# Performance work log

Measured on AMD Instinct MI355X. Metric: run time of the kernel, lower is better.

## Reference

```python
import jax, jax.numpy as jnp
import numpy as np

B, S, DIM = 2, 2048, 2048
NH = 16
Q_LORA, KV_LORA = 1536, 512
NOPE, ROPE, VHD = 128, 64, 128
QK_HD = NOPE + ROPE  # 192
EPS = 1e-6
SCALE = QK_HD ** -0.5


def rmsnorm(x, w, eps=EPS):
    return x * jax.lax.rsqrt(jnp.mean(x * x, axis=-1, keepdims=True) + eps) * w


def apply_rope(x, cos, sin):
    # x: (b, s, h, d) with d even; cos/sin: (s, d//2)
    xr, xi = x[..., 0::2], x[..., 1::2]
    c = cos[None, :, None, :]
    s = sin[None, :, None, :]
    yr = xr * c - xi * s
    yi = xr * s + xi * c
    return jnp.stack([yr, yi], axis=-1).reshape(x.shape)


def setup_inputs() -> dict:
    key = jax.random.key(0)
    ks = jax.random.split(key, 12)
    std = 0.02
    # RoPE tables (unit-magnitude complex as cos/sin)
    inv_freq = 1.0 / (10000.0 ** (np.arange(0, ROPE, 2, dtype=np.float32) / ROPE))  # (32,)
    ang = np.arange(S, dtype=np.float32)[:, None] * inv_freq[None, :]  # (S, 32)
    return {
        "x": jax.random.normal(ks[0], (B, S, DIM), jnp.float32),
        "freqs_cos": jnp.asarray(np.cos(ang)),
        "freqs_sin": jnp.asarray(np.sin(ang)),
        "wq_a_w": jax.random.normal(ks[1], (Q_LORA, DIM), jnp.float32) * std,
        "wq_a_b": jnp.zeros((Q_LORA,), jnp.float32),
        "q_norm_w": jnp.ones((Q_LORA,), jnp.float32),
        "wq_b_w": jax.random.normal(ks[2], (NH * QK_HD, Q_LORA), jnp.float32) * std,
        "wq_b_b": jnp.zeros((NH * QK_HD,), jnp.float32),
        "wkv_a_w": jax.random.normal(ks[3], (KV_LORA + ROPE, DIM), jnp.float32) * std,
        "wkv_a_b": jnp.zeros((KV_LORA + ROPE,), jnp.float32),
        "kv_norm_w": jnp.ones((KV_LORA,), jnp.float32),
        "wkv_b_w": jax.random.normal(ks[4], (NH * (NOPE + VHD), KV_LORA), jnp.float32) * std,
        "wkv_b_b": jnp.zeros((NH * (NOPE + VHD),), jnp.float32),
        "wo_w": jax.random.normal(ks[5], (DIM, NH * VHD), jnp.float32) * std,
        "wo_b": jnp.zeros((DIM,), jnp.float32),
    }


def reference(x, freqs_cos, freqs_sin, wq_a_w, wq_a_b, q_norm_w, wq_b_w, wq_b_b,
              wkv_a_w, wkv_a_b, kv_norm_w, wkv_b_w, wkv_b_b, wo_w, wo_b):
    b, s, _ = x.shape
    # Low-rank Q projection: wq_b(q_norm(wq_a(x)))
    q = rmsnorm(x @ wq_a_w.T + wq_a_b, q_norm_w) @ wq_b_w.T + wq_b_b
    q = q.reshape(b, s, NH, QK_HD)
    q_nope, q_pe = q[..., :NOPE], q[..., NOPE:]
    q = jnp.concatenate([q_nope, apply_rope(q_pe, freqs_cos, freqs_sin)], axis=-1)
    # Low-rank KV projection
    kv = x @ wkv_a_w.T + wkv_a_b  # (b, s, kv_lora + rope)
    kv_c, k_pe = kv[..., :KV_LORA], kv[..., KV_LORA:]
    k_pe = apply_rope(k_pe[:, :, None, :], freqs_cos, freqs_sin)  # (b, s, 1, rope)
    kv = rmsnorm(kv_c, kv_norm_w) @ wkv_b_w.T + wkv_b_b
    kv = kv.reshape(b, s, NH, NOPE + VHD)
    k_nope, v = kv[..., :NOPE], kv[..., NOPE:]
    k = jnp.concatenate([k_nope, jnp.broadcast_to(k_pe, (b, s, NH, ROPE))], axis=-1)
    # Causal SDPA
    scores = jnp.einsum("bqhd,bkhd->bhqk", q, k) * SCALE
    causal = jnp.tril(jnp.ones((s, s), bool))
    scores = jnp.where(causal[None, None], scores, jnp.float32(-1e30))
    attn = jax.nn.softmax(scores, axis=-1)
    out = jnp.einsum("bhqk,bkhd->bqhd", attn, v).reshape(b, s, NH * VHD)
    return out @ wo_w.T + wo_b
```

## Files before the change

kernel.cpp:

```cpp
#include <hip/hip_runtime.h>


typedef __bf16 bf16x8 __attribute__((ext_vector_type(8)));
typedef float f32x4 __attribute__((ext_vector_type(4)));
typedef unsigned short u16;

#define SEQ 2048
#define SCALE 0.07216878364870323f
#define NEGBIG -30000.0f

__device__ __forceinline__ float b2f(u16 u) {
  union { unsigned u; float f; } c; c.u = ((unsigned)u) << 16; return c.f;
}
__device__ __forceinline__ u16 f2b(float f) {
  union { float f; unsigned u; } c; c.f = f;
  unsigned r = (c.u + 0x7fffu + ((c.u >> 16) & 1u)) >> 16;
  return (u16)r;
}
__device__ __forceinline__ uint4 pack8(float4 a, float4 b) {
  union { uint4 v; u16 e[8]; } t;
  t.e[0] = f2b(a.x); t.e[1] = f2b(a.y); t.e[2] = f2b(a.z); t.e[3] = f2b(a.w);
  t.e[4] = f2b(b.x); t.e[5] = f2b(b.y); t.e[6] = f2b(b.z); t.e[7] = f2b(b.w);
  return t.v;
}

__global__ void cvt_kernel(const float* __restrict__ src, u16* __restrict__ dst,
                           long n8) {
  long i = (long)blockIdx.x * 256 + threadIdx.x;
  long stride = (long)gridDim.x * 256;
  for (; i < n8; i += stride) {
    const float4* s = (const float4*)(src + i * 8);
    float4 a = s[0], b = s[1];
    *(uint4*)(dst + i * 8) = pack8(a, b);
  }
}

template <int XF, int WF, int OF>
__global__ __launch_bounds__(256, 3) void gemm_kernel(
    const void* __restrict__ X, int lda, const void* __restrict__ W,
    const float* __restrict__ bias, void* __restrict__ out,
    int M, int N, int K, float oscale) {
  constexpr int LDT = 72;
  __shared__ alignas(16) u16 As[64 * LDT];
  __shared__ alignas(16) u16 Bs[128 * LDT];
  const int tid = threadIdx.x;
  const int wave = tid >> 6, lane = tid & 63;
  const int quad = lane >> 4, l16 = lane & 15;
  const int bm = blockIdx.x * 64, bn = blockIdx.y * 128;
  const int wn = wave * 32;
  const int srow = tid >> 3;
  const int scol = (tid & 7) * 8;

  f32x4 acc[4][2] = {};

  float4 pa32[2][2], pb32[4][2];
  uint4  pa16[2],    pb16[4];

  auto load_tile = [&](int k0) {
#pragma unroll
    for (int p = 0; p < 2; ++p) {
      size_t off = (size_t)(bm + srow + p * 32) * lda + k0 + scol;
      if (XF) {
        const float* s = (const float*)X + off;
        pa32[p][0] = *(const float4*)s;
        pa32[p][1] = *(const float4*)(s + 4);
      } else {
        pa16[p] = *(const uint4*)((const u16*)X + off);
      }
    }
#pragma unroll
    for (int p = 0; p < 4; ++p) {
      int n = bn + srow + p * 32;
      size_t off = (size_t)n * K + k0 + scol;
      if (WF) {
        if (n < N) {
          const float* s = (const float*)W + off;
          pb32[p][0] = *(const float4*)s;
          pb32[p][1] = *(const float4*)(s + 4);
        } else {
          pb32[p][0] = make_float4(0.f, 0.f, 0.f, 0.f);
          pb32[p][1] = make_float4(0.f, 0.f, 0.f, 0.f);
        }
      } else {
        if (n < N) pb16[p] = *(const uint4*)((const u16*)W + off);
        else { pb16[p].x = pb16[p].y = pb16[p].z = pb16[p].w = 0u; }
      }
    }
  };

  load_tile(0);
  for (int k0 = 0; k0 < K; k0 += 64) {
    __syncthreads();
#pragma unroll
    for (int p = 0; p < 2; ++p) {
      uint4 v;
      if (XF) v = pack8(pa32[p][0], pa32[p][1]); else v = pa16[p];
      *(uint4*)(&As[(srow + p * 32) * LDT + scol]) = v;
    }
#pragma unroll
    for (int p = 0; p < 4; ++p) {
      uint4 v;
      if (WF) v = pack8(pb32[p][0], pb32[p][1]); else v = pb16[p];
      *(uint4*)(&Bs[(srow + p * 32) * LDT + scol]) = v;
    }
    __syncthreads();
    if (k0 + 64 < K) load_tile(k0 + 64);

#pragma unroll
    for (int kk = 0; kk < 64; kk += 32) {
      bf16x8 a[4], b[2];
#pragma unroll
      for (int i = 0; i < 4; ++i)
        a[i] = *(const bf16x8*)(&As[(i * 16 + l16) * LDT + kk + quad * 8]);
#pragma unroll
      for (int j = 0; j < 2; ++j)
        b[j] = *(const bf16x8*)(&Bs[(wn + j * 16 + l16) * LDT + kk + quad * 8]);
#pragma unroll
      for (int i = 0; i < 4; ++i)
#pragma unroll
        for (int j = 0; j < 2; ++j)
          acc[i][j] = __builtin_amdgcn_mfma_f32_16x16x32_bf16(a[i], b[j], acc[i][j], 0, 0, 0);
    }
  }

#pragma unroll
  for (int i = 0; i < 4; ++i)
#pragma unroll
    for (int j = 0; j < 2; ++j) {
      int col = bn + wn + j * 16 + l16;
      if (col < N) {
        float bv = bias[col];
#pragma unroll
        for (int r = 0; r < 4; ++r) {
          int row = bm + i * 16 + quad * 4 + r;
          float v = (acc[i][j][r] + bv) * oscale;
          if (OF) ((float*)out)[(size_t)row * N + col] = v;
          else    ((u16*)out)[(size_t)row * N + col] = f2b(v);
        }
      }
    }
}

__global__ void rmsnorm_kernel(u16* x, const float* __restrict__ w,
                               int C, int stride) {
  size_t base = (size_t)blockIdx.x * stride;
  float s = 0.f;
  for (int c = threadIdx.x; c < C; c += 256) { float v = b2f(x[base + c]); s += v * v; }
#pragma unroll
  for (int off = 32; off > 0; off >>= 1) s += __shfl_xor(s, off, 64);
  __shared__ float red[4];
  if ((threadIdx.x & 63) == 0) red[threadIdx.x >> 6] = s;
  __syncthreads();
  float tot = red[0] + red[1] + red[2] + red[3];
  float scale = rsqrtf(tot / (float)C + 1e-6f);
  for (int c = threadIdx.x; c < C; c += 256)
    x[base + c] = f2b(b2f(x[base + c]) * scale * w[c]);
}

__global__ void rope_kpe_kernel(const u16* __restrict__ kvn,
                                const float* __restrict__ fcos,
                                const float* __restrict__ fsin,
                                u16* __restrict__ kpe) {
  int idx = blockIdx.x * 256 + threadIdx.x;
  int t = idx >> 5, i = idx & 31;
  int s = t & (SEQ - 1);
  float c = fcos[s * 32 + i], sn = fsin[s * 32 + i];
  float xr = b2f(kvn[(size_t)t * 576 + 512 + 2 * i]);
  float xi = b2f(kvn[(size_t)t * 576 + 512 + 2 * i + 1]);
  kpe[(size_t)t * 64 + 2 * i]     = f2b(xr * c - xi * sn);
  kpe[(size_t)t * 64 + 2 * i + 1] = f2b(xr * sn + xi * c);
}

__global__ void rope_q_kernel(u16* q, const float* __restrict__ fcos,
                              const float* __restrict__ fsin) {
  int idx = blockIdx.x * 256 + threadIdx.x;
  int t = idx >> 8, h = (idx >> 5) & 7, i = idx & 31;
  int s = t & (SEQ - 1);
  float c = fcos[s * 32 + i], sn = fsin[s * 32 + i];
  size_t base = (size_t)t * 1536 + h * 192 + 128 + 2 * i;
  float xr = b2f(q[base]), xi = b2f(q[base + 1]);
  q[base]     = f2b(xr * c - xi * sn);
  q[base + 1] = f2b(xr * sn + xi * c);
}

template <int PAIRED>
__global__ __launch_bounds__(256, 2) void attn_kernel(
    const u16* __restrict__ Q0,
    const u16* __restrict__ Q1,
    const u16* __restrict__ KV0,
    const u16* __restrict__ KV1,
    const u16* __restrict__ KPE,
    u16* __restrict__ O,
    int hbase) {
  constexpr int LK = 200;
  constexpr int LP = 72;
  __shared__ alignas(16) u16 Ks[64 * LK];
  __shared__ alignas(16) u16 Ps[64 * LP];
  __shared__ alignas(16) u16 Vs[128 * LP];

  const int tid = threadIdx.x;
  const int wave = tid >> 6, lane = tid & 63;
  const int quad = lane >> 4, l16 = lane & 15;
  const int h = hbase + blockIdx.y;
  const int hl = h & 7;
  const u16* __restrict__ Q   = (h & 8) ? Q1  : Q0;
  const u16* __restrict__ KVB = (h & 8) ? KV1 : KV0;
  const size_t tok0 = (size_t)blockIdx.z * SEQ;

  auto process = [&](int qt) {
    const int q0 = qt * 64;
    bf16x8 qf[6];
    {
      const u16* qp = Q + (tok0 + q0 + wave * 16 + l16) * 1536 + hl * 192 + quad * 8;
#pragma unroll
      for (int c = 0; c < 6; ++c) qf[c] = *(const bf16x8*)(qp + c * 32);
    }

    f32x4 o_acc[8] = {};
    float m_i[4], l_i[4];
#pragma unroll
    for (int r = 0; r < 4; ++r) { m_i[r] = NEGBIG; l_i[r] = 0.f; }

    const int nkt = qt + 1;
    uint4 kreg[6], vreg[4];
    auto load_tile = [&](int kt) {
      int k0 = kt * 64;
#pragma unroll
      for (int p = 0; p < 6; ++p) {
        int flat = tid + p * 256;
        int r = flat / 24, c8 = (flat % 24) * 8;
        const u16* src = (c8 < 128)
            ? (KVB + (tok0 + k0 + r) * 2048 + hl * 256 + c8)
            : (KPE + (tok0 + k0 + r) * 64 + (c8 - 128));
        kreg[p] = *(const uint4*)src;
      }
#pragma unroll
      for (int p = 0; p < 4; ++p) {
        int flat = tid + p * 256;
        int r = flat / 16, c8 = (flat % 16) * 8;
        vreg[p] = *(const uint4*)(KVB + (tok0 + k0 + r) * 2048 + hl * 256 + 128 + c8);
      }
    };

    load_tile(0);
    for (int kt = 0; kt < nkt; ++kt) {
      const int k0 = kt * 64;
      __syncthreads();
#pragma unroll
      for (int p = 0; p < 6; ++p) {
        int flat = tid + p * 256;
        int r = flat / 24, c8 = (flat % 24) * 8;
        *(uint4*)(&Ks[r * LK + c8]) = kreg[p];
      }
#pragma unroll
      for (int p = 0; p < 4; ++p) {
        int flat = tid + p * 256;
        int r = flat / 16, c8 = (flat % 16) * 8;
        union { uint4 v4; u16 e[8]; } t;
        t.v4 = vreg[p];
        int rs = r >> 3, rl = r & 7;
#pragma unroll
        for (int j = 0; j < 8; ++j) {
          int n = c8 + j;
          Vs[n * LP + ((rs ^ ((n >> 3) & 7)) << 3) + rl] = t.e[j];
        }
      }
      __syncthreads();
      if (kt + 1 < nkt) load_tile(kt + 1);

      f32x4 sc[4];
#pragma unroll
      for (int ni = 0; ni < 4; ++ni) {
        f32x4 a = {};
#pragma unroll
        for (int c = 0; c < 6; ++c) {
          bf16x8 kf = *(const bf16x8*)(&Ks[(ni * 16 + l16) * LK + c * 32 + quad * 8]);
          a = __builtin_amdgcn_mfma_f32_16x16x32_bf16(qf[c], kf, a, 0, 0, 0);
        }
        sc[ni] = a;
      }

      const int qrow_base = q0 + wave * 16 + quad * 4;
      if (kt == nkt - 1) {
#pragma unroll
        for (int ni = 0; ni < 4; ++ni) {
          int col = k0 + ni * 16 + l16;
#pragma unroll
          for (int r = 0; r < 4; ++r)
            if (col > qrow_base + r) sc[ni][r] = NEGBIG;
        }
      }

      float mloc[4];
#pragma unroll
      for (int r = 0; r < 4; ++r) mloc[r] = NEGBIG;
#pragma unroll
      for (int ni = 0; ni < 4; ++ni)
#pragma unroll
        for (int r = 0; r < 4; ++r) mloc[r] = fmaxf(mloc[r], sc[ni][r]);
#pragma unroll
      for (int off = 1; off < 16; off <<= 1)
#pragma unroll
        for (int r = 0; r < 4; ++r) mloc[r] = fmaxf(mloc[r], __shfl_xor(mloc[r], off, 64));

      float alpha[4], rsum[4];
#pragma unroll
      for (int r = 0; r < 4; ++r) {
        float mn = fmaxf(m_i[r], mloc[r]);
        alpha[r] = __expf(m_i[r] - mn);
        m_i[r] = mn;
        rsum[r] = 0.f;
      }
#pragma unroll
      for (int ni = 0; ni < 4; ++ni)
#pragma unroll
        for (int r = 0; r < 4; ++r) {
          float p = __expf(sc[ni][r] - m_i[r]);
          sc[ni][r] = p;
          rsum[r] += p;
        }
#pragma unroll
      for (int off = 1; off < 16; off <<= 1)
#pragma unroll
        for (int r = 0; r < 4; ++r) rsum[r] += __shfl_xor(rsum[r], off, 64);
#pragma unroll
      for (int r = 0; r < 4; ++r) l_i[r] = l_i[r] * alpha[r] + rsum[r];

#pragma unroll
      for (int ni = 0; ni < 4; ++ni)
#pragma unroll
        for (int r = 0; r < 4; ++r)
          Ps[(wave * 16 + quad * 4 + r) * LP + ni * 16 + l16] = f2b(sc[ni][r]);

      __syncthreads();

#pragma unroll
      for (int t8 = 0; t8 < 8; ++t8)
#pragma unroll
        for (int r = 0; r < 4; ++r) o_acc[t8][r] *= alpha[r];

      bf16x8 pf0 = *(const bf16x8*)(&Ps[(wave * 16 + l16) * LP + quad * 8]);
      bf16x8 pf1 = *(const bf16x8*)(&Ps[(wave * 16 + l16) * LP + 32 + quad * 8]);
#pragma unroll
      for (int ni = 0; ni < 8; ++ni) {
        int n0 = ni * 16 + l16;
        int sw = (n0 >> 3) & 7;
        bf16x8 vf0 = *(const bf16x8*)(&Vs[n0 * LP + ((quad ^ sw) << 3)]);
        bf16x8 vf1 = *(const bf16x8*)(&Vs[n0 * LP + (((4 + quad) ^ sw) << 3)]);
        o_acc[ni] = __builtin_amdgcn_mfma_f32_16x16x32_bf16(pf0, vf0, o_acc[ni], 0, 0, 0);
        o_acc[ni] = __builtin_amdgcn_mfma_f32_16x16x32_bf16(pf1, vf1, o_acc[ni], 0, 0, 0);
      }
    }

#pragma unroll
    for (int ni = 0; ni < 8; ++ni) {
      int col = h * 128 + ni * 16 + l16;
#pragma unroll
      for (int r = 0; r < 4; ++r) {
        size_t row = tok0 + q0 + wave * 16 + quad * 4 + r;
        O[row * 2048 + col] = f2b(o_acc[ni][r] / l_i[r]);
      }
    }
  };

  if (PAIRED) {
    process(31 - (int)blockIdx.x);
    process((int)blockIdx.x);
  } else {
    process(blockIdx.z == 0 ? (31 - (int)blockIdx.x) : (int)blockIdx.x);
  }
}

extern "C" void kernel_launch(void* const* d_in, const int* in_sizes, int n_in,
                              void* d_out, int out_size, void* d_ws, size_t ws_size,
                              hipStream_t stream) {
  const float* x      = (const float*)d_in[0];
  const float* fcos   = (const float*)d_in[1];
  const float* fsin   = (const float*)d_in[2];
  const float* wqa    = (const float*)d_in[3];
  const float* wqa_b  = (const float*)d_in[4];
  const float* qnw    = (const float*)d_in[5];
  const float* wqb    = (const float*)d_in[6];
  const float* wqb_b  = (const float*)d_in[7];
  const float* wkva   = (const float*)d_in[8];
  const float* wkva_b = (const float*)d_in[9];
  const float* kvnw   = (const float*)d_in[10];
  const float* wkvb   = (const float*)d_in[11];
  const float* wkvb_b = (const float*)d_in[12];
  const float* wo     = (const float*)d_in[13];
  const float* wo_b   = (const float*)d_in[14];

  char* ws = (char*)d_ws;
  u16* qn   = (u16*)(ws + 0);
  u16* kvn  = (u16*)(ws + 12582912);
  u16* kpe  = (u16*)(ws + 17301504);
  u16* qbA  = (u16*)(ws + 17825792);
  u16* kvB  = (u16*)(ws + 30408704);
  u16* ao   = (u16*)(ws + 47185920);

  dim3 blk(256);

  if (ws_size >= 123994112u) {
    u16* xb    = (u16*)(ws + 63963136);
    u16* kvA   = (u16*)(ws + 63963136);
    u16* wqab  = (u16*)(ws + 80740352);
    u16* wkvab = (u16*)(ws + 87031808);
    u16* wqbb  = (u16*)(ws + 89391104);
    u16* wkvbw = (u16*)(ws + 98828288);
    u16* wob   = (u16*)(ws + 103022592);
    u16* qbB   = (u16*)(ws + 111411200);

    cvt_kernel<<<2048, blk, 0, stream>>>(x,    xb,    1048576);
    cvt_kernel<<<1536, blk, 0, stream>>>(wqa,  wqab,   393216);
    cvt_kernel<<< 576, blk, 0, stream>>>(wkva, wkvab,  147456);
    cvt_kernel<<<2048, blk, 0, stream>>>(wqb,  wqbb,   589824);
    cvt_kernel<<<1024, blk, 0, stream>>>(wkvb, wkvbw,  262144);
    cvt_kernel<<<2048, blk, 0, stream>>>(wo,   wob,    524288);

    gemm_kernel<0,0,0><<<dim3(64, 12), blk, 0, stream>>>(xb, 2048, wqab, wqa_b, qn, 4096, 1536, 2048, 1.0f);
    gemm_kernel<0,0,0><<<dim3(64, 5),  blk, 0, stream>>>(xb, 2048, wkvab, wkva_b, kvn, 4096, 576, 2048, 1.0f);
    rmsnorm_kernel<<<4096, blk, 0, stream>>>(qn, qnw, 1536, 1536);
    rmsnorm_kernel<<<4096, blk, 0, stream>>>(kvn, kvnw, 512, 576);
    rope_kpe_kernel<<<512, blk, 0, stream>>>(kvn, fcos, fsin, kpe);

    gemm_kernel<0,0,0><<<dim3(64, 12), blk, 0, stream>>>(qn, 1536, wqbb, wqb_b, qbA, 4096, 1536, 1536, SCALE);
    gemm_kernel<0,0,0><<<dim3(64, 12), blk, 0, stream>>>(qn, 1536, wqbb + (size_t)1536 * 1536, wqb_b + 1536, qbB, 4096, 1536, 1536, SCALE);
    rope_q_kernel<<<4096, blk, 0, stream>>>(qbA, fcos, fsin);
    rope_q_kernel<<<4096, blk, 0, stream>>>(qbB, fcos, fsin);
    gemm_kernel<0,0,0><<<dim3(64, 16), blk, 0, stream>>>(kvn, 576, wkvbw, wkvb_b, kvA, 4096, 2048, 512, 1.0f);
    gemm_kernel<0,0,0><<<dim3(64, 16), blk, 0, stream>>>(kvn, 576, wkvbw + (size_t)2048 * 512, wkvb_b + 2048, kvB, 4096, 2048, 512, 1.0f);

    attn_kernel<1><<<dim3(16, 16, 2), blk, 0, stream>>>(qbA, qbB, kvA, kvB, kpe, ao, 0);

    gemm_kernel<0,0,1><<<dim3(64, 16), blk, 0, stream>>>(ao, 2048, wob, wo_b, (float*)d_out, 4096, 2048, 2048, 1.0f);
  } else if (ws_size >= 111411200u) {
    u16* xb    = (u16*)(ws + 63963136);
    u16* wqab  = (u16*)(ws + 80740352);
    u16* wkvab = (u16*)(ws + 87031808);
    u16* wqbb  = (u16*)(ws + 89391104);
    u16* wkvbw = (u16*)(ws + 98828288);
    u16* wob   = (u16*)(ws + 103022592);

    cvt_kernel<<<2048, blk, 0, stream>>>(x,    xb,    1048576);
    cvt_kernel<<<1536, blk, 0, stream>>>(wqa,  wqab,   393216);
    cvt_kernel<<< 576, blk, 0, stream>>>(wkva, wkvab,  147456);
    cvt_kernel<<<2048, blk, 0, stream>>>(wqb,  wqbb,   589824);
    cvt_kernel<<<1024, blk, 0, stream>>>(wkvb, wkvbw,  262144);
    cvt_kernel<<<2048, blk, 0, stream>>>(wo,   wob,    524288);

    gemm_kernel<0,0,0><<<dim3(64, 12), blk, 0, stream>>>(xb, 2048, wqab, wqa_b, qn, 4096, 1536, 2048, 1.0f);
    gemm_kernel<0,0,0><<<dim3(64, 5),  blk, 0, stream>>>(xb, 2048, wkvab, wkva_b, kvn, 4096, 576, 2048, 1.0f);
    rmsnorm_kernel<<<4096, blk, 0, stream>>>(qn, qnw, 1536, 1536);
    rmsnorm_kernel<<<4096, blk, 0, stream>>>(kvn, kvnw, 512, 576);
    rope_kpe_kernel<<<512, blk, 0, stream>>>(kvn, fcos, fsin, kpe);

    for (int g = 0; g < 2; ++g) {
      const u16* wqb_g   = wqbb + (size_t)g * 1536 * 1536;
      const float* wqb_bg  = wqb_b + g * 1536;
      const u16* wkvb_g  = wkvbw + (size_t)g * 2048 * 512;
      const float* wkvb_bg = wkvb_b + g * 2048;
      gemm_kernel<0,0,0><<<dim3(64, 12), blk, 0, stream>>>(qn, 1536, wqb_g, wqb_bg, qbA, 4096, 1536, 1536, SCALE);
      rope_q_kernel<<<4096, blk, 0, stream>>>(qbA, fcos, fsin);
      gemm_kernel<0,0,0><<<dim3(64, 16), blk, 0, stream>>>(kvn, 576, wkvb_g, wkvb_bg, kvB, 4096, 2048, 512, 1.0f);
      attn_kernel<0><<<dim3(32, 8, 2), blk, 0, stream>>>(qbA, qbA, kvB, kvB, kpe, ao, g * 8);
    }

    gemm_kernel<0,0,1><<<dim3(64, 16), blk, 0, stream>>>(ao, 2048, wob, wo_b, (float*)d_out, 4096, 2048, 2048, 1.0f);
  } else {
    gemm_kernel<1,1,0><<<dim3(64, 12), blk, 0, stream>>>(x, 2048, wqa, wqa_b, qn, 4096, 1536, 2048, 1.0f);
    gemm_kernel<1,1,0><<<dim3(64, 5),  blk, 0, stream>>>(x, 2048, wkva, wkva_b, kvn, 4096, 576, 2048, 1.0f);
    rmsnorm_kernel<<<4096, blk, 0, stream>>>(qn, qnw, 1536, 1536);
    rmsnorm_kernel<<<4096, blk, 0, stream>>>(kvn, kvnw, 512, 576);
    rope_kpe_kernel<<<512, blk, 0, stream>>>(kvn, fcos, fsin, kpe);

    for (int g = 0; g < 2; ++g) {
      const float* wqb_g   = wqb + (size_t)g * 1536 * 1536;
      const float* wqb_bg  = wqb_b + g * 1536;
      const float* wkvb_g  = wkvb + (size_t)g * 2048 * 512;
      const float* wkvb_bg = wkvb_b + g * 2048;
      gemm_kernel<0,1,0><<<dim3(64, 12), blk, 0, stream>>>(qn, 1536, wqb_g, wqb_bg, qbA, 4096, 1536, 1536, SCALE);
      rope_q_kernel<<<4096, blk, 0, stream>>>(qbA, fcos, fsin);
      gemm_kernel<0,1,0><<<dim3(64, 16), blk, 0, stream>>>(kvn, 576, wkvb_g, wkvb_bg, kvB, 4096, 2048, 512, 1.0f);
      attn_kernel<0><<<dim3(32, 8, 2), blk, 0, stream>>>(qbA, qbA, kvB, kvB, kpe, ao, g * 8);
    }

    gemm_kernel<0,1,1><<<dim3(64, 16), blk, 0, stream>>>(ao, 2048, wo, wo_b, (float*)d_out, 4096, 2048, 2048, 1.0f);
  }
}
```

Measured before the change: 577.4 us.

## Add 128x128 double-buffered GEMM using direct global-to-LDS loads with swizzle

Introduces a new bf16 GEMM kernel with 128x128 tiles, four waves each computing a 64x64 sub-tile, and double-buffered LDS staging through global_load_lds so loads bypass registers. An XOR swizzle on the column index avoids LDS bank conflicts. It replaces the older 64x128 GEMM for most projections, aiming for more reuse per tile and overlap of loads with MFMA work. In exchange it uses more LDS and launches fewer blocks, which can lower occupancy, and it relies on M and N being multiples of 128.

```diff
diff --git a/kernel.cpp b/kernel.cpp
--- a/kernel.cpp
+++ b/kernel.cpp
@@ -23,6 +23,11 @@
   t.e[4] = f2b(b.x); t.e[5] = f2b(b.y); t.e[6] = f2b(b.z); t.e[7] = f2b(b.w);
   return t.v;
 }
+
+#define GLOAD_LDS16(gsrc, ldst)                                              \
+  __builtin_amdgcn_global_load_lds(                                          \
+      (const __attribute__((address_space(1))) unsigned int*)(gsrc),         \
+      (__attribute__((address_space(3))) unsigned int*)(ldst), 16, 0, 0)
 
 __global__ void cvt_kernel(const float* __restrict__ src, u16* __restrict__ dst,
                            long n8) {
@@ -33,6 +38,79 @@
     float4 a = s[0], b = s[1];
     *(uint4*)(dst + i * 8) = pack8(a, b);
   }
+}
+
+template <int OF>
+__global__ __launch_bounds__(256) void gemm_lds_kernel(
+    const u16* __restrict__ X, int lda, const u16* __restrict__ W,
+    const float* __restrict__ bias, void* __restrict__ out,
+    int N, int K, float oscale) {
+  __shared__ alignas(16) u16 As[2][128 * 64];
+  __shared__ alignas(16) u16 Bs[2][128 * 64];
+  const int tid = threadIdx.x;
+  const int wave = tid >> 6, lane = tid & 63;
+  const int quad = lane >> 4, l16 = lane & 15;
+  const int wr = (wave >> 1) * 64, wc = (wave & 1) * 64;
+  const int bm = blockIdx.x * 128, bn = blockIdx.y * 128;
+  const int srow0 = wave * 32 + (lane >> 3);
+  const int gcol = ((lane & 7) ^ (lane >> 3)) * 8;
+
+  f32x4 acc[4][4] = {};
+
+  auto stage = [&](int buf, int k0) {
+#pragma unroll
+    for (int p = 0; p < 4; ++p) {
+      int row = srow0 + p * 8;
+      const u16* ga = X + (size_t)(bm + row) * lda + k0 + gcol;
+      const u16* gb = W + (size_t)(bn + row) * K + k0 + gcol;
+      char* la = (char*)(&As[buf][0]) + (wave * 4 + p) * 1024;
+      char* lb = (char*)(&Bs[buf][0]) + (wave * 4 + p) * 1024;
+      GLOAD_LDS16(ga, la);
+      GLOAD_LDS16(gb, lb);
+    }
+  };
+
+  const int nk = K >> 6;
+  stage(0, 0);
+  int cur = 0;
+  for (int kt = 0; kt < nk; ++kt) {
+    __syncthreads();
+    if (kt + 1 < nk) stage(cur ^ 1, (kt + 1) * 64);
+    const u16* as = &As[cur][0];
+    const u16* bs = &Bs[cur][0];
+#pragma unroll
+    for (int kk = 0; kk < 64; kk += 32) {
+      const int cs = (kk + quad * 8) ^ ((l16 & 7) * 8);
+      bf16x8 a[4], b[4];
+#pragma unroll
+      for (int i = 0; i < 4; ++i)
+        a[i] = *(const bf16x8*)(as + (wr + i * 16 + l16) * 64 + cs);
+#pragma unroll
+      for (int j = 0; j < 4; ++j)
+        b[j] = *(const bf16x8*)(bs + (wc + j * 16 + l16) * 64 + cs);
+#pragma unroll
+      for (int i = 0; i < 4; ++i)
+#pragma unroll
+        for (int j = 0; j < 4; ++j)
+          acc[i][j] = __builtin_amdgcn_mfma_f32_16x16x32_bf16(a[i], b[j], acc[i][j], 0, 0, 0);
+    }
+    cur ^= 1;
+  }
+
+#pragma unroll
+  for (int i = 0; i < 4; ++i)
+#pragma unroll
+    for (int j = 0; j < 4; ++j) {
+      int col = bn + wc + j * 16 + l16;
+      float bv = bias[col];
+#pragma unroll
+      for (int r = 0; r < 4; ++r) {
+        int row = bm + wr + i * 16 + quad * 4 + r;
+        float v = (acc[i][j][r] + bv) * oscale;
+        if (OF) ((float*)out)[(size_t)row * N + col] = v;
+        else    ((u16*)out)[(size_t)row * N + col] = f2b(v);
+      }
+    }
 }
 
 template <int XF, int WF, int OF>
@@ -417,22 +495,22 @@
     cvt_kernel<<<1024, blk, 0, stream>>>(wkvb, wkvbw,  262144);
     cvt_kernel<<<2048, blk, 0, stream>>>(wo,   wob,    524288);
 
-    gemm_kernel<0,0,0><<<dim3(64, 12), blk, 0, stream>>>(xb, 2048, wqab, wqa_b, qn, 4096, 1536, 2048, 1.0f);
+    gemm_lds_kernel<0><<<dim3(32, 12), blk, 0, stream>>>(xb, 2048, wqab, wqa_b, qn, 1536, 2048, 1.0f);
     gemm_kernel<0,0,0><<<dim3(64, 5),  blk, 0, stream>>>(xb, 2048, wkvab, wkva_b, kvn, 4096, 576, 2048, 1.0f);
     rmsnorm_kernel<<<4096, blk, 0, stream>>>(qn, qnw, 1536, 1536);
     rmsnorm_kernel<<<4096, blk, 0, stream>>>(kvn, kvnw, 512, 576);
     rope_kpe_kernel<<<512, blk, 0, stream>>>(kvn, fcos, fsin, kpe);
 
-    gemm_kernel<0,0,0><<<dim3(64, 12), blk, 0, stream>>>(qn, 1536, wqbb, wqb_b, qbA, 4096, 1536, 1536, SCALE);
-    gemm_kernel<0,0,0><<<dim3(64, 12), blk, 0, stream>>>(qn, 1536, wqbb + (size_t)1536 * 1536, wqb_b + 1536, qbB, 4096, 1536, 1536, SCALE);
+    gemm_lds_kernel<0><<<dim3(32, 12), blk, 0, stream>>>(qn, 1536, wqbb, wqb_b, qbA, 1536, 1536, SCALE);
+    gemm_lds_kernel<0><<<dim3(32, 12), blk, 0, stream>>>(qn, 1536, wqbb + (size_t)1536 * 1536, wqb_b + 1536, qbB, 1536, 1536, SCALE);
     rope_q_kernel<<<4096, blk, 0, stream>>>(qbA, fcos, fsin);
     rope_q_kernel<<<4096, blk, 0, stream>>>(qbB, fcos, fsin);
-    gemm_kernel<0,0,0><<<dim3(64, 16), blk, 0, stream>>>(kvn, 576, wkvbw, wkvb_b, kvA, 4096, 2048, 512, 1.0f);
-    gemm_kernel<0,0,0><<<dim3(64, 16), blk, 0, stream>>>(kvn, 576, wkvbw + (size_t)2048 * 512, wkvb_b + 2048, kvB, 4096, 2048, 512, 1.0f);
+    gemm_lds_kernel<0><<<dim3(32, 16), blk, 0, stream>>>(kvn, 576, wkvbw, wkvb_b, kvA, 2048, 512, 1.0f);
+    gemm_lds_kernel<0><<<dim3(32, 16), blk, 0, stream>>>(kvn, 576, wkvbw + (size_t)2048 * 512, wkvb_b + 2048, kvB, 2048, 512, 1.0f);
 
     attn_kernel<1><<<dim3(16, 16, 2), blk, 0, stream>>>(qbA, qbB, kvA, kvB, kpe, ao, 0);
 
-    gemm_kernel<0,0,1><<<dim3(64, 16), blk, 0, stream>>>(ao, 2048, wob, wo_b, (float*)d_out, 4096, 2048, 2048, 1.0f);
+    gemm_lds_kernel<1><<<dim3(32, 16), blk, 0, stream>>>(ao, 2048, wob, wo_b, (float*)d_out, 2048, 2048, 1.0f);
   } else if (ws_size >= 111411200u) {
     u16* xb    = (u16*)(ws + 63963136);
     u16* wqab  = (u16*)(ws + 80740352);
```

New measurement: 546.1 us. 5.4% less time.
